# Kernel optimization log

Measured on AMD Instinct MI355X. Metric: run time of the kernel, lower is better.

## Reference

```python
import jax, jax.numpy as jnp
import numpy as np
from jax import lax

T, B, HW, HID, NA = 128, 64, 52, 512, 15  # rollout len, num_envs, image size, lstm hidden, n_actions


def setup_inputs() -> dict:
    key = jax.random.key(0)
    ks = jax.random.split(key, 20)
    BT = T * B
    x = jax.random.uniform(ks[0], (BT, HW, HW, 3), dtype=jnp.float32) * 255.0
    done = jax.random.randint(ks[1], (BT,), 0, 2).astype(jnp.float32)
    h0 = jax.random.normal(ks[2], (B, HID), dtype=jnp.float32) * 0.1
    c0 = jax.random.normal(ks[3], (B, HID), dtype=jnp.float32) * 0.1
    action = jax.random.randint(ks[4], (BT,), 0, NA, dtype=jnp.int32)
    n = lambda k, s, sc: jax.random.normal(k, s, dtype=jnp.float32) * sc
    return {
        "x": x, "done": done, "h0": h0, "c0": c0, "action": action,
        "conv_w1": n(ks[5], (32, 3, 8, 8), 0.05), "conv_b1": jnp.zeros((32,), jnp.float32),
        "conv_w2": n(ks[6], (64, 32, 4, 4), 0.05), "conv_b2": jnp.zeros((64,), jnp.float32),
        "conv_w3": n(ks[7], (64, 64, 3, 3), 0.05), "conv_b3": jnp.zeros((64,), jnp.float32),
        "fc_w": n(ks[8], (576, HID), 0.05), "fc_b": jnp.zeros((HID,), jnp.float32),
        "w_ih": n(ks[9], (4 * HID, HID), 0.04), "w_hh": n(ks[10], (4 * HID, HID), 0.04),
        "b_lstm": jnp.zeros((4 * HID,), jnp.float32),
        "actor_w": n(ks[11], (HID, NA), 0.01), "actor_b": jnp.zeros((NA,), jnp.float32),
        "critic_w": n(ks[12], (HID, 1), 0.05), "critic_b": jnp.zeros((1,), jnp.float32),
    }


def _conv(x, w, b, stride):
    y = lax.conv_general_dilated(x, w, (stride, stride), "VALID",
                                 dimension_numbers=("NCHW", "OIHW", "NCHW"))
    return y + b[None, :, None, None]


def _forward(x, done, h0, c0, conv_w1, conv_b1, conv_w2, conv_b2, conv_w3, conv_b3,
             fc_w, fc_b, w_ih, w_hh, b_lstm, actor_w, actor_b, critic_w, critic_b, action):
    # CNN encoder (input arrives NHWC like the torch caller, permute to NCHW)
    z = jnp.transpose(x, (0, 3, 1, 2)) / 255.0
    z = jax.nn.relu(_conv(z, conv_w1, conv_b1, 4))   # [BT,32,12,12]
    z = jax.nn.relu(_conv(z, conv_w2, conv_b2, 2))   # [BT,64,5,5]
    z = jax.nn.relu(_conv(z, conv_w3, conv_b3, 1))   # [BT,64,3,3]
    z = z.reshape(z.shape[0], -1)                    # [BT,576]
    hidden = jax.nn.relu(z @ fc_w + fc_b)            # [BT,512]

    seq = hidden.reshape(T, B, HID)
    dseq = done.reshape(T, B)

    def step(carry, inp):
        h, c = carry
        xt, dt = inp
        m = (1.0 - dt)[:, None]                       # done-mask resets state
        h, c = h * m, c * m
        gates = xt @ w_ih.T + h @ w_hh.T + b_lstm     # [B,4H], gate order i,f,g,o
        i, f, g, o = jnp.split(gates, 4, axis=-1)
        i, f, o = jax.nn.sigmoid(i), jax.nn.sigmoid(f), jax.nn.sigmoid(o)
        c = f * c + i * jnp.tanh(g)
        h = o * jnp.tanh(c)
        return (h, c), h

    (hT, cT), hs = lax.scan(step, (h0, c0), (seq, dseq))
    feats = hs.reshape(T * B, HID)

    logits = feats @ actor_w + actor_b               # [BT,NA]
    logp = jax.nn.log_softmax(logits)
    lp_a = jnp.take_along_axis(logp, action[:, None], axis=1)[:, 0]
    entropy = -jnp.sum(jnp.exp(logp) * logp, axis=-1)
    value = feats @ critic_w + critic_b              # [BT,1]
    return lp_a, entropy, value, hT, cT


def reference(x, done, h0, c0, conv_w1, conv_b1, conv_w2, conv_b2, conv_w3, conv_b3,
              fc_w, fc_b, w_ih, w_hh, b_lstm, actor_w, actor_b, critic_w, critic_b, action):
    return _forward(x, done, h0, c0, conv_w1, conv_b1, conv_w2, conv_b2, conv_w3, conv_b3,
                    fc_w, fc_b, w_ih, w_hh, b_lstm, actor_w, actor_b, critic_w, critic_b, action)
```

## Files before the change

### kernel.cpp

```cpp
#include <hip/hip_runtime.h>
#include <hip/hip_bf16.h>
#include <math.h>

typedef unsigned short u16;
typedef __attribute__((ext_vector_type(8))) short bf16x8;
typedef __attribute__((ext_vector_type(4))) float f32x4;

__device__ inline u16 f2b(float f) {
  __hip_bfloat16 h = __float2bfloat16(f);
  return *(u16*)&h;
}

__global__ void __launch_bounds__(256) prep_k(
    const float* __restrict__ w1, const float* __restrict__ w2,
    const float* __restrict__ w3, const float* __restrict__ fcw,
    const float* __restrict__ whh, const float* __restrict__ done,
    const float* __restrict__ h0, const float* __restrict__ c0,
    u16* __restrict__ w1bh, u16* __restrict__ w2bh, u16* __restrict__ w3bh,
    u16* __restrict__ fcwT, float* __restrict__ whhT,
    float* __restrict__ hT0, float* __restrict__ cbuf) {
  int i = blockIdx.x * 256 + threadIdx.x;
  if (i < 8192) {
    int c = i >> 8, k = i & 255;
    int ky = k >> 5, rem = k & 31;
    float v = 0.f;
    if (rem < 24) {
      int kx = rem / 3, ch = rem - kx * 3;
      v = w1[((c * 3 + ch) * 8 + ky) * 8 + kx] * (1.0f / 255.0f);
    }
    w1bh[i] = f2b(v);
    return;
  }
  i -= 8192;
  if (i < 32768) {
    int c = i >> 9, k = i & 511;
    int ci = k & 31, kyx = k >> 5;
    int ky = kyx >> 2, kx = kyx & 3;
    w2bh[i] = f2b(w2[c * 512 + ci * 16 + ky * 4 + kx]);
    return;
  }
  i -= 32768;
  if (i < 36864) {
    int c = i / 576, k = i - c * 576;
    int ci = k & 63, kyx = k >> 6;
    int ky = kyx / 3, kx = kyx - ky * 3;
    w3bh[i] = f2b(w3[((c * 64 + ci) * 3 + ky) * 3 + kx]);
    return;
  }
  i -= 36864;
  if (i < 294912) {
    int o = i / 576, r = i - o * 576;
    int c = r & 63, yx = r >> 6;
    fcwT[i] = f2b(fcw[(c * 9 + yx) * 512 + o]);
    return;
  }
  i -= 294912;
  if (i < 1048576) {
    int j = i & 2047, k = i >> 11;
    whhT[i] = whh[j * 512 + k];
    return;
  }
  i -= 1048576;
  if (i < 32768) {
    int b = i & 63;
    int k = i >> 6;
    hT0[i] = h0[b * 512 + k] * (1.0f - done[b]);
    return;
  }
  i -= 32768;
  if (i < 32768) {
    int b = i >> 9;
    cbuf[i] = c0[i] * (1.0f - done[b]);
  }
}

__global__ void __launch_bounds__(256) conv1m_k(
    const float* __restrict__ x, const u16* __restrict__ w1bh,
    const float* __restrict__ b1, u16* __restrict__ a1h) {
  __shared__ u16 As[256 * 40];
  __shared__ u16 Bs[32 * 40];
  const int tid = threadIdx.x;
  const long bm = (long)blockIdx.x * 256;
  const int w = tid >> 6;
  const int lane = tid & 63;
  const int lr = lane & 15;
  const int lk = lane >> 4;
  const int wm = w * 64;
  const int r = (int)bm + tid;
  const int n = r / 144;
  const int p = r - n * 144;
  const int py = p / 12;
  const int px = p - py * 12;
  const long gbase = (long)n * 8112 + py * 624 + px * 12;
  f32x4 zero = {0.f, 0.f, 0.f, 0.f};
  f32x4 acc[4][2];
#pragma unroll
  for (int mi = 0; mi < 4; ++mi)
#pragma unroll
    for (int ni = 0; ni < 2; ++ni) acc[mi][ni] = zero;

  const ushort4 z4 = {0, 0, 0, 0};
  for (int ky = 0; ky < 8; ++ky) {
    const float* src = x + gbase + ky * 156;
    float4 v[6];
#pragma unroll
    for (int q = 0; q < 6; ++q) v[q] = *(const float4*)&src[q * 4];
    u16* dst = &As[tid * 40];
#pragma unroll
    for (int q = 0; q < 6; ++q) {
      ushort4 o;
      o.x = f2b(v[q].x); o.y = f2b(v[q].y);
      o.z = f2b(v[q].z); o.w = f2b(v[q].w);
      *(ushort4*)&dst[q * 4] = o;
    }
    *(ushort4*)&dst[24] = z4;
    *(ushort4*)&dst[28] = z4;
    if (tid < 128) {
      const int c = tid >> 2, q = tid & 3;
      *(uint4*)&Bs[c * 40 + q * 8] = *(const uint4*)&w1bh[c * 256 + ky * 32 + q * 8];
    }
    __syncthreads();
    bf16x8 af[4], bfr[2];
#pragma unroll
    for (int mi = 0; mi < 4; ++mi)
      af[mi] = *(const bf16x8*)&As[(wm + mi * 16 + lr) * 40 + lk * 8];
#pragma unroll
    for (int ni = 0; ni < 2; ++ni)
      bfr[ni] = *(const bf16x8*)&Bs[(ni * 16 + lr) * 40 + lk * 8];
#pragma unroll
    for (int mi = 0; mi < 4; ++mi)
#pragma unroll
      for (int ni = 0; ni < 2; ++ni)
        acc[mi][ni] = __builtin_amdgcn_mfma_f32_16x16x32_bf16(
            af[mi], bfr[ni], acc[mi][ni], 0, 0, 0);
    __syncthreads();
  }
#pragma unroll
  for (int ni = 0; ni < 2; ++ni) {
    float bv = b1[ni * 16 + lr];
#pragma unroll
    for (int mi = 0; mi < 4; ++mi) {
#pragma unroll
      for (int j = 0; j < 4; ++j) {
        long rg = bm + wm + mi * 16 + lk * 4 + j;
        float v = fmaxf(acc[mi][ni][j] + bv, 0.f);
        a1h[rg * 32 + ni * 16 + lr] = f2b(v);
      }
    }
  }
}

__global__ void __launch_bounds__(256) conv2m_k(
    const u16* __restrict__ a1h, const u16* __restrict__ w2bh,
    const float* __restrict__ b2, u16* __restrict__ a2h) {
  __shared__ u16 As[256 * 40];
  __shared__ u16 Bs[64 * 40];
  const int tid = threadIdx.x;
  const long bm = (long)blockIdx.x * 256;
  const int w = tid >> 6;
  const int lane = tid & 63;
  const int lr = lane & 15;
  const int lk = lane >> 4;
  const int wm = w * 64;
  const int r = (int)bm + tid;
  const int n = r / 25;
  const int p = r - n * 25;
  const int py = p / 5;
  const int px = p - py * 5;
  const int pbase = n * 4608 + (py * 24 + px * 2) * 32;
  f32x4 zero = {0.f, 0.f, 0.f, 0.f};
  f32x4 acc[4][4];
#pragma unroll
  for (int mi = 0; mi < 4; ++mi)
#pragma unroll
    for (int ni = 0; ni < 4; ++ni) acc[mi][ni] = zero;

  for (int ks = 0; ks < 16; ++ks) {
    const int koff = ((ks >> 2) * 12 + (ks & 3)) * 32;
#pragma unroll
    for (int q = 0; q < 4; ++q)
      *(uint4*)&As[tid * 40 + q * 8] = *(const uint4*)&a1h[pbase + koff + q * 8];
    {
      const int c = tid >> 2, q = tid & 3;
      *(uint4*)&Bs[c * 40 + q * 8] = *(const uint4*)&w2bh[c * 512 + ks * 32 + q * 8];
    }
    __syncthreads();
    bf16x8 af[4], bfr[4];
#pragma unroll
    for (int mi = 0; mi < 4; ++mi)
      af[mi] = *(const bf16x8*)&As[(wm + mi * 16 + lr) * 40 + lk * 8];
#pragma unroll
    for (int ni = 0; ni < 4; ++ni)
      bfr[ni] = *(const bf16x8*)&Bs[(ni * 16 + lr) * 40 + lk * 8];
#pragma unroll
    for (int mi = 0; mi < 4; ++mi)
#pragma unroll
      for (int ni = 0; ni < 4; ++ni)
        acc[mi][ni] = __builtin_amdgcn_mfma_f32_16x16x32_bf16(
            af[mi], bfr[ni], acc[mi][ni], 0, 0, 0);
    __syncthreads();
  }
#pragma unroll
  for (int ni = 0; ni < 4; ++ni) {
    float bv = b2[ni * 16 + lr];
#pragma unroll
    for (int mi = 0; mi < 4; ++mi) {
#pragma unroll
      for (int j = 0; j < 4; ++j) {
        long rg = bm + wm + mi * 16 + lk * 4 + j;
        float v = fmaxf(acc[mi][ni][j] + bv, 0.f);
        a2h[rg * 64 + ni * 16 + lr] = f2b(v);
      }
    }
  }
}

__global__ void __launch_bounds__(256) conv3m_k(
    const u16* __restrict__ a2h, const u16* __restrict__ w3bh,
    const float* __restrict__ b3, u16* __restrict__ a3h) {
  __shared__ u16 As[256 * 40];
  __shared__ u16 Bs[64 * 40];
  const int tid = threadIdx.x;
  const long bm = (long)blockIdx.x * 256;
  const int w = tid >> 6;
  const int lane = tid & 63;
  const int lr = lane & 15;
  const int lk = lane >> 4;
  const int wm = w * 64;
  const int r = (int)bm + tid;
  const int n = r / 9;
  const int p = r - n * 9;
  const int py = p / 3;
  const int px = p - py * 3;
  const int pbase = n * 1600 + (py * 5 + px) * 64;
  f32x4 zero = {0.f, 0.f, 0.f, 0.f};
  f32x4 acc[4][4];
#pragma unroll
  for (int mi = 0; mi < 4; ++mi)
#pragma unroll
    for (int ni = 0; ni < 4; ++ni) acc[mi][ni] = zero;

  for (int ks2 = 0; ks2 < 18; ++ks2) {
    const int tap = ks2 >> 1;
    const int ky = tap / 3, kx = tap - ky * 3;
    const int koff = (ky * 5 + kx) * 64 + (ks2 & 1) * 32;
#pragma unroll
    for (int q = 0; q < 4; ++q)
      *(uint4*)&As[tid * 40 + q * 8] = *(const uint4*)&a2h[pbase + koff + q * 8];
    {
      const int c = tid >> 2, q = tid & 3;
      *(uint4*)&Bs[c * 40 + q * 8] = *(const uint4*)&w3bh[c * 576 + ks2 * 32 + q * 8];
    }
    __syncthreads();
    bf16x8 af[4], bfr[4];
#pragma unroll
    for (int mi = 0; mi < 4; ++mi)
      af[mi] = *(const bf16x8*)&As[(wm + mi * 16 + lr) * 40 + lk * 8];
#pragma unroll
    for (int ni = 0; ni < 4; ++ni)
      bfr[ni] = *(const bf16x8*)&Bs[(ni * 16 + lr) * 40 + lk * 8];
#pragma unroll
    for (int mi = 0; mi < 4; ++mi)
#pragma unroll
      for (int ni = 0; ni < 4; ++ni)
        acc[mi][ni] = __builtin_amdgcn_mfma_f32_16x16x32_bf16(
            af[mi], bfr[ni], acc[mi][ni], 0, 0, 0);
    __syncthreads();
  }
#pragma unroll
  for (int ni = 0; ni < 4; ++ni) {
    float bv = b3[ni * 16 + lr];
#pragma unroll
    for (int mi = 0; mi < 4; ++mi) {
#pragma unroll
      for (int j = 0; j < 4; ++j) {
        long rg = bm + wm + mi * 16 + lk * 4 + j;
        float v = fmaxf(acc[mi][ni][j] + bv, 0.f);
        a3h[rg * 64 + ni * 16 + lr] = f2b(v);
      }
    }
  }
}

__global__ void __launch_bounds__(256) cast_k(
    const float4* __restrict__ wihv, ushort4* __restrict__ wihh) {
  int i = blockIdx.x * 256 + threadIdx.x;
  if (i < 262144) {
    float4 v = wihv[i];
    ushort4 o;
    o.x = f2b(v.x); o.y = f2b(v.y); o.z = f2b(v.z); o.w = f2b(v.w);
    wihh[i] = o;
  }
}

__global__ void __launch_bounds__(256) mgemm_k(
    const u16* __restrict__ A, const u16* __restrict__ B,
    const float* __restrict__ bias, float* __restrict__ Cf,
    u16* __restrict__ Ch, const int K, const int N,
    const int RELU, const int OUTBF16) {
  __shared__ u16 As[128 * 40];
  __shared__ u16 Bs[128 * 40];
  const int tid = threadIdx.x;
  const long bm = (long)blockIdx.x * 128;
  const long bn = (long)blockIdx.y * 128;
  const int w = tid >> 6;
  const int lane = tid & 63;
  const int lr = lane & 15;
  const int lk = lane >> 4;
  const int wm = (w >> 1) * 64, wn = (w & 1) * 64;
  f32x4 zero = {0.f, 0.f, 0.f, 0.f};
  f32x4 acc[4][4];
#pragma unroll
  for (int mi = 0; mi < 4; ++mi)
#pragma unroll
    for (int ni = 0; ni < 4; ++ni) acc[mi][ni] = zero;

  for (int k0 = 0; k0 < K; k0 += 32) {
#pragma unroll
    for (int q = 0; q < 2; ++q) {
      int idx = tid * 2 + q;
      int row = idx >> 2, kq = (idx & 3) * 8;
      *(uint4*)&As[row * 40 + kq] = *(const uint4*)&A[(bm + row) * K + k0 + kq];
      *(uint4*)&Bs[row * 40 + kq] = *(const uint4*)&B[(bn + row) * K + k0 + kq];
    }
    __syncthreads();
    bf16x8 af[4], bfr[4];
#pragma unroll
    for (int mi = 0; mi < 4; ++mi)
      af[mi] = *(const bf16x8*)&As[(wm + mi * 16 + lr) * 40 + lk * 8];
#pragma unroll
    for (int ni = 0; ni < 4; ++ni)
      bfr[ni] = *(const bf16x8*)&Bs[(wn + ni * 16 + lr) * 40 + lk * 8];
#pragma unroll
    for (int mi = 0; mi < 4; ++mi)
#pragma unroll
      for (int ni = 0; ni < 4; ++ni)
        acc[mi][ni] = __builtin_amdgcn_mfma_f32_16x16x32_bf16(
            af[mi], bfr[ni], acc[mi][ni], 0, 0, 0);
    __syncthreads();
  }
#pragma unroll
  for (int ni = 0; ni < 4; ++ni) {
    float bv = bias[bn + wn + ni * 16 + lr];
#pragma unroll
    for (int mi = 0; mi < 4; ++mi) {
#pragma unroll
      for (int j = 0; j < 4; ++j) {
        long rg = bm + wm + mi * 16 + lk * 4 + j;
        long cg = bn + wn + ni * 16 + lr;
        float v = acc[mi][ni][j] + bv;
        if (RELU) v = fmaxf(v, 0.f);
        if (OUTBF16) Ch[rg * N + cg] = f2b(v);
        else Cf[rg * N + cg] = v;
      }
    }
  }
}

__global__ void __launch_bounds__(512) lstm_step_k(
    const float* __restrict__ gx, const float* __restrict__ whhT,
    const float* __restrict__ done, float* __restrict__ hT2,
    float* __restrict__ cbuf, float* __restrict__ hseq,
    float* __restrict__ outh, float* __restrict__ outc, const int t) {
  __shared__ float red[512][37];
  const int tid = threadIdx.x;
  const int bid = blockIdx.x;
  const int uslice = (bid & 7) * 4 + (bid >> 6);
  const int bg = (bid >> 3) & 7;
  const int uu = tid & 15;
  const int kc = tid >> 4;
  const int u = uslice * 16 + uu;
  const int b0 = bg * 8;
  const int fbl = tid >> 4;

  const float* hTp = hT2 + (t & 1) * 32768;
  float a0[8] = {0.f}, a1_[8] = {0.f}, a2_[8] = {0.f}, a3_[8] = {0.f};
  const int kbeg = kc * 16;
#pragma unroll 4
  for (int kk = 0; kk < 16; ++kk) {
    int k = kbeg + kk;
    const float* wr = whhT + k * 2048;
    float w0 = wr[u];
    float w1 = wr[u + 512];
    float w2 = wr[u + 1024];
    float w3 = wr[u + 1536];
    float hv[8];
    *(float4*)&hv[0] = *(const float4*)&hTp[k * 64 + b0];
    *(float4*)&hv[4] = *(const float4*)&hTp[k * 64 + b0 + 4];
#pragma unroll
    for (int j = 0; j < 8; ++j) {
      a0[j] += w0 * hv[j]; a1_[j] += w1 * hv[j];
      a2_[j] += w2 * hv[j]; a3_[j] += w3 * hv[j];
    }
  }
#pragma unroll
  for (int j = 0; j < 8; ++j) {
    red[tid][j] = a0[j];       red[tid][8 + j] = a1_[j];
    red[tid][16 + j] = a2_[j]; red[tid][24 + j] = a3_[j];
  }
  __syncthreads();
  if (fbl < 8) {
    float s0 = 0.f, s1 = 0.f, s2 = 0.f, s3 = 0.f;
#pragma unroll
    for (int q = 0; q < 32; ++q) {
      const float* rp = red[q * 16 + uu];
      s0 += rp[fbl]; s1 += rp[8 + fbl]; s2 += rp[16 + fbl]; s3 += rp[24 + fbl];
    }
    const int b = b0 + fbl;
    const int ug = uslice * 16 + uu;
    const int row = t * 64 + b;
    const float* gxr = gx + (long)row * 2048;
    float pi = s0 + gxr[ug];
    float pf = s1 + gxr[512 + ug];
    float pg_ = s2 + gxr[1024 + ug];
    float po = s3 + gxr[1536 + ug];
    float ig = 1.f / (1.f + expf(-pi));
    float fg = 1.f / (1.f + expf(-pf));
    float og = 1.f / (1.f + expf(-po));
    float gg = tanhf(pg_);
    float cn = fg * cbuf[b * 512 + ug] + ig * gg;
    float hn = og * tanhf(cn);
    hseq[(long)row * 512 + ug] = hn;
    if (t == 127) {
      outh[b * 512 + ug] = hn;
      outc[b * 512 + ug] = cn;
    } else {
      float mn = 1.f - done[(t + 1) * 64 + b];
      cbuf[b * 512 + ug] = cn * mn;
      hT2[((t + 1) & 1) * 32768 + ug * 64 + b] = hn * mn;
    }
  }
}

__global__ void __launch_bounds__(256) heads_k(
    const float* __restrict__ hseq, const float* __restrict__ aw,
    const float* __restrict__ ab, const float* __restrict__ cw,
    const float* __restrict__ cb, const int* __restrict__ action,
    float* __restrict__ out) {
  const int lane = threadIdx.x & 63;
  const int wid = threadIdx.x >> 6;
  const int row = blockIdx.x * 4 + wid;
  const int j = lane & 15;
  const int kc = lane >> 4;
  const float* f = hseq + (long)row * 512;
  float acc = 0.f;
  if (j < 15) {
    for (int k = kc * 128; k < kc * 128 + 128; ++k) acc += f[k] * aw[k * 15 + j];
  } else {
    for (int k = kc * 128; k < kc * 128 + 128; ++k) acc += f[k] * cw[k];
  }
  acc += __shfl_xor(acc, 16);
  acc += __shfl_xor(acc, 32);
  float logit = (j < 15) ? acc + ab[j] : -1e30f;
  float m = logit;
#pragma unroll
  for (int off = 1; off < 16; off <<= 1) m = fmaxf(m, __shfl_xor(m, off));
  float p = (j < 15) ? expf(logit - m) : 0.f;
  float S = p;
#pragma unroll
  for (int off = 1; off < 16; off <<= 1) S += __shfl_xor(S, off);
  float logS = logf(S);
  float lp = logit - m - logS;
  float e = (j < 15) ? p * lp : 0.f;
  float es = e;
#pragma unroll
  for (int off = 1; off < 16; off <<= 1) es += __shfl_xor(es, off);
  float ent = -es / S;
  int a = action[row];
  float lpa = __shfl(lp, (lane & 48) | a);
  float val = __shfl(acc, (lane & 48) | 15) + cb[0];
  if (lane == 0) {
    out[row] = lpa;
    out[8192 + row] = ent;
    out[16384 + row] = val;
  }
}

extern "C" void kernel_launch(void* const* d_in, const int* in_sizes, int n_in,
                              void* d_out, int out_size, void* d_ws, size_t ws_size,
                              hipStream_t stream) {
  const float* x    = (const float*)d_in[0];
  const float* done = (const float*)d_in[1];
  const float* h0   = (const float*)d_in[2];
  const float* c0   = (const float*)d_in[3];
  const int*   act  = (const int*)d_in[4];
  const float* w1   = (const float*)d_in[5];
  const float* b1   = (const float*)d_in[6];
  const float* w2   = (const float*)d_in[7];
  const float* b2   = (const float*)d_in[8];
  const float* w3   = (const float*)d_in[9];
  const float* b3   = (const float*)d_in[10];
  const float* fcw  = (const float*)d_in[11];
  const float* fcb  = (const float*)d_in[12];
  const float* wih  = (const float*)d_in[13];
  const float* whh  = (const float*)d_in[14];
  const float* blst = (const float*)d_in[15];
  const float* aw   = (const float*)d_in[16];
  const float* ab   = (const float*)d_in[17];
  const float* cw   = (const float*)d_in[18];
  const float* cb   = (const float*)d_in[19];
  float* ws  = (float*)d_ws;
  float* out = (float*)d_out;

  u16*  a1h   = (u16*)ws;
  u16*  wihh  = (u16*)(ws + 4718592);
  float* hseq = ws + 8912896;
  u16*  a2h   = (u16*)(ws + 37748736);
  u16*  a3h   = (u16*)(ws + 44302336);
  u16*  hidh  = (u16*)(ws + 46661632);
  float* gxb  = ws + 50855936;
  u16*  w1bh  = (u16*)(ws + 67633152);
  u16*  w2bh  = (u16*)(ws + 67639296);
  u16*  w3bh  = (u16*)(ws + 67672064);
  u16*  fcwT  = (u16*)(ws + 67708928);
  float* whhT = ws + 68003840;
  float* hT2  = ws + 69052416;
  float* cbuf = ws + 69117952;

  hipLaunchKernelGGL(prep_k, dim3(5808), dim3(256), 0, stream,
                     w1, w2, w3, fcw, whh, done, h0, c0,
                     w1bh, w2bh, w3bh, fcwT, whhT, hT2, cbuf);
  hipLaunchKernelGGL(conv1m_k, dim3(4608), dim3(256), 0, stream, x, w1bh, b1, a1h);
  hipLaunchKernelGGL(conv2m_k, dim3(800), dim3(256), 0, stream, a1h, w2bh, b2, a2h);
  hipLaunchKernelGGL(conv3m_k, dim3(288), dim3(256), 0, stream, a2h, w3bh, b3, a3h);
  hipLaunchKernelGGL(cast_k, dim3(1024), dim3(256), 0, stream,
                     (const float4*)wih, (ushort4*)wihh);
  hipLaunchKernelGGL(mgemm_k, dim3(64, 4), dim3(256), 0, stream,
                     a3h, fcwT, fcb, (float*)nullptr, hidh, 576, 512, 1, 1);
  hipLaunchKernelGGL(mgemm_k, dim3(64, 16), dim3(256), 0, stream,
                     hidh, wihh, blst, gxb, (u16*)nullptr, 512, 2048, 0, 0);
  for (int t = 0; t < 128; ++t) {
    hipLaunchKernelGGL(lstm_step_k, dim3(256), dim3(512), 0, stream,
                       gxb, whhT, done, hT2, cbuf, hseq,
                       out + 24576, out + 57344, t);
  }
  hipLaunchKernelGGL(heads_k, dim3(2048), dim3(256), 0, stream,
                     hseq, aw, ab, cw, cb, act, out);
}
```

Baseline: 1.224 ms.

## Fuse LSTM time steps into one persistent cooperative kernel with grid barrier

Replaces 128 per-timestep LSTM kernel launches with a single cooperative persistent kernel that loops over time. Blocks synchronise through a two-level atomic tree barrier, and the hidden state is exchanged via agent-scope atomic loads and stores in a double buffer. This removes per-step launch overhead and the implicit inter-kernel sync, at the cost of spin-wait barrier latency and relying on all 256 blocks being co-resident. It falls back to the per-step launches if the cooperative launch fails.

```diff
diff --git a/kernel.cpp b/kernel.cpp
--- a/kernel.cpp
+++ b/kernel.cpp
@@ -18,7 +18,8 @@
     const float* __restrict__ h0, const float* __restrict__ c0,
     u16* __restrict__ w1bh, u16* __restrict__ w2bh, u16* __restrict__ w3bh,
     u16* __restrict__ fcwT, float* __restrict__ whhT,
-    float* __restrict__ hT0, float* __restrict__ cbuf) {
+    float* __restrict__ hT0, float* __restrict__ cbuf,
+    int* __restrict__ bar) {
   int i = blockIdx.x * 256 + threadIdx.x;
   if (i < 8192) {
     int c = i >> 8, k = i & 255;
@@ -71,7 +72,10 @@
   if (i < 32768) {
     int b = i >> 9;
     cbuf[i] = c0[i] * (1.0f - done[b]);
-  }
+    return;
+  }
+  i -= 32768;
+  if (i < 2048) bar[i] = 0;
 }
 
 __global__ void __launch_bounds__(256) conv1m_k(
@@ -353,6 +357,120 @@
         if (OUTBF16) Ch[rg * N + cg] = f2b(v);
         else Cf[rg * N + cg] = v;
       }
+    }
+  }
+}
+
+__global__ void __launch_bounds__(512) lstm_all_k(
+    const float* __restrict__ gx, const float* __restrict__ whhT,
+    const float* __restrict__ done, float* __restrict__ hT2,
+    float* __restrict__ cbuf, float* __restrict__ hseq,
+    float* __restrict__ outh, float* __restrict__ outc,
+    int* __restrict__ bar) {
+  __shared__ float red[512][37];
+  const int tid = threadIdx.x;
+  const int bid = blockIdx.x;
+  const int uslice = (bid & 7) * 4 + (bid >> 6);
+  const int bg = (bid >> 3) & 7;
+  const int uu = tid & 15;
+  const int kc = tid >> 4;
+  const int u = uslice * 16 + uu;
+  const int b0 = bg * 8;
+  const int fbl = tid >> 4;
+  const int kbeg = kc * 16;
+  const int leaf = bid & 15;
+
+  for (int t = 0; t < 128; ++t) {
+    const float* hTp = hT2 + (t & 1) * 32768;
+    float a0[8] = {0.f}, a1_[8] = {0.f}, a2_[8] = {0.f}, a3_[8] = {0.f};
+#pragma unroll 4
+    for (int kk = 0; kk < 16; ++kk) {
+      int k = kbeg + kk;
+      const float* wr = whhT + k * 2048;
+      float w0 = wr[u];
+      float w1 = wr[u + 512];
+      float w2 = wr[u + 1024];
+      float w3 = wr[u + 1536];
+      union { unsigned long long q[4]; float f[8]; } hu;
+      const unsigned long long* hp =
+          (const unsigned long long*)(hTp + k * 64 + b0);
+      hu.q[0] = __hip_atomic_load(hp + 0, __ATOMIC_RELAXED, __HIP_MEMORY_SCOPE_AGENT);
+      hu.q[1] = __hip_atomic_load(hp + 1, __ATOMIC_RELAXED, __HIP_MEMORY_SCOPE_AGENT);
+      hu.q[2] = __hip_atomic_load(hp + 2, __ATOMIC_RELAXED, __HIP_MEMORY_SCOPE_AGENT);
+      hu.q[3] = __hip_atomic_load(hp + 3, __ATOMIC_RELAXED, __HIP_MEMORY_SCOPE_AGENT);
+#pragma unroll
+      for (int j = 0; j < 8; ++j) {
+        a0[j] += w0 * hu.f[j]; a1_[j] += w1 * hu.f[j];
+        a2_[j] += w2 * hu.f[j]; a3_[j] += w3 * hu.f[j];
+      }
+    }
+#pragma unroll
+    for (int j = 0; j < 8; ++j) {
+      red[tid][j] = a0[j];       red[tid][8 + j] = a1_[j];
+      red[tid][16 + j] = a2_[j]; red[tid][24 + j] = a3_[j];
+    }
+    __syncthreads();
+    if (fbl < 8) {
+      float s0 = 0.f, s1 = 0.f, s2 = 0.f, s3 = 0.f;
+#pragma unroll
+      for (int q = 0; q < 32; ++q) {
+        const float* rp = red[q * 16 + uu];
+        s0 += rp[fbl]; s1 += rp[8 + fbl]; s2 += rp[16 + fbl]; s3 += rp[24 + fbl];
+      }
+      const int b = b0 + fbl;
+      const int ug = uslice * 16 + uu;
+      const int row = t * 64 + b;
+      const float* gxr = gx + (long)row * 2048;
+      float pi = s0 + gxr[ug];
+      float pf = s1 + gxr[512 + ug];
+      float pg_ = s2 + gxr[1024 + ug];
+      float po = s3 + gxr[1536 + ug];
+      float ig = 1.f / (1.f + expf(-pi));
+      float fg = 1.f / (1.f + expf(-pf));
+      float og = 1.f / (1.f + expf(-po));
+      float gg = tanhf(pg_);
+      float cn = fg * cbuf[b * 512 + ug] + ig * gg;
+      float hn = og * tanhf(cn);
+      hseq[(long)row * 512 + ug] = hn;
+      if (t == 127) {
+        outh[b * 512 + ug] = hn;
+        outc[b * 512 + ug] = cn;
+      } else {
+        float mn = 1.f - done[(t + 1) * 64 + b];
+        cbuf[b * 512 + ug] = cn * mn;
+        __hip_atomic_store(&hT2[((t + 1) & 1) * 32768 + ug * 64 + b], hn * mn,
+                           __ATOMIC_RELAXED, __HIP_MEMORY_SCOPE_AGENT);
+      }
+    }
+    if (t < 127) {
+      __syncthreads();
+      if (tid == 0) {
+        int prev = __hip_atomic_fetch_add(&bar[leaf * 32], 1,
+                                          __ATOMIC_ACQ_REL, __HIP_MEMORY_SCOPE_AGENT);
+        if (prev == 15) {
+          __hip_atomic_store(&bar[leaf * 32], 0,
+                             __ATOMIC_RELAXED, __HIP_MEMORY_SCOPE_AGENT);
+          int rprev = __hip_atomic_fetch_add(&bar[512], 1,
+                                             __ATOMIC_ACQ_REL, __HIP_MEMORY_SCOPE_AGENT);
+          if (rprev == 15) {
+            __hip_atomic_store(&bar[512], 0,
+                               __ATOMIC_RELAXED, __HIP_MEMORY_SCOPE_AGENT);
+            __hip_atomic_store(&bar[544], t + 1,
+                               __ATOMIC_RELEASE, __HIP_MEMORY_SCOPE_AGENT);
+          } else {
+            while (__hip_atomic_load(&bar[544], __ATOMIC_RELAXED,
+                                     __HIP_MEMORY_SCOPE_AGENT) <= t)
+              __builtin_amdgcn_s_sleep(2);
+          }
+          __hip_atomic_store(&bar[576 + leaf * 32], t + 1,
+                             __ATOMIC_RELAXED, __HIP_MEMORY_SCOPE_AGENT);
+        } else {
+          while (__hip_atomic_load(&bar[576 + leaf * 32], __ATOMIC_RELAXED,
+                                   __HIP_MEMORY_SCOPE_AGENT) <= t)
+            __builtin_amdgcn_s_sleep(2);
+        }
+      }
+      __syncthreads();
     }
   }
 }
@@ -516,10 +634,11 @@
   float* whhT = ws + 68003840;
   float* hT2  = ws + 69052416;
   float* cbuf = ws + 69117952;
-
-  hipLaunchKernelGGL(prep_k, dim3(5808), dim3(256), 0, stream,
+  int*  bar   = (int*)(ws + 69150720);
+
+  hipLaunchKernelGGL(prep_k, dim3(5816), dim3(256), 0, stream,
                      w1, w2, w3, fcw, whh, done, h0, c0,
-                     w1bh, w2bh, w3bh, fcwT, whhT, hT2, cbuf);
+                     w1bh, w2bh, w3bh, fcwT, whhT, hT2, cbuf, bar);
   hipLaunchKernelGGL(conv1m_k, dim3(4608), dim3(256), 0, stream, x, w1bh, b1, a1h);
   hipLaunchKernelGGL(conv2m_k, dim3(800), dim3(256), 0, stream, a1h, w2bh, b2, a2h);
   hipLaunchKernelGGL(conv3m_k, dim3(288), dim3(256), 0, stream, a2h, w3bh, b3, a3h);
@@ -529,10 +648,22 @@
                      a3h, fcwT, fcb, (float*)nullptr, hidh, 576, 512, 1, 1);
   hipLaunchKernelGGL(mgemm_k, dim3(64, 16), dim3(256), 0, stream,
                      hidh, wihh, blst, gxb, (u16*)nullptr, 512, 2048, 0, 0);
-  for (int t = 0; t < 128; ++t) {
-    hipLaunchKernelGGL(lstm_step_k, dim3(256), dim3(512), 0, stream,
-                       gxb, whhT, done, hT2, cbuf, hseq,
-                       out + 24576, out + 57344, t);
+  {
+    const float* gxp = gxb; const float* whhTp = whhT; const float* dp = done;
+    float* hT2p = hT2; float* cbp = cbuf; float* hsp = hseq;
+    float* ohp = out + 24576; float* ocp = out + 57344; int* barp = bar;
+    void* args[] = {(void*)&gxp, (void*)&whhTp, (void*)&dp, (void*)&hT2p,
+                    (void*)&cbp, (void*)&hsp, (void*)&ohp, (void*)&ocp,
+                    (void*)&barp};
+    hipError_t err = hipLaunchCooperativeKernel((void*)lstm_all_k, dim3(256),
+                                                dim3(512), args, 0, stream);
+    if (err != hipSuccess) {
+      for (int t = 0; t < 128; ++t) {
+        hipLaunchKernelGGL(lstm_step_k, dim3(256), dim3(512), 0, stream,
+                           gxb, whhT, done, hT2, cbuf, hseq,
+                           out + 24576, out + 57344, t);
+      }
+    }
   }
   hipLaunchKernelGGL(heads_k, dim3(2048), dim3(256), 0, stream,
                      hseq, aw, ab, cw, cb, act, out);
```

Result: slower. 2.345 ms (+91.5%).
